# Performance work log

Hardware: AMD Instinct MI355X
Metric: run time of the kernel (lower is better)

## Reference

```python
import jax, jax.numpy as jnp
import numpy as np

BATCH, C, IMG, P = 32, 3, 224, 32
G = IMG // P            # 7
N = G * G               # 49 patches
E, NH, L = 768, 12, 12
DH = E // NH
DFF, MLP, NC = 3072, 2048, 5
FLAT = (N + 1 + L) * E  # 62*768 = 47616


def setup_inputs() -> dict:
    key = jax.random.key(0)
    ks = iter(jax.random.split(key, 32))
    nrm = lambda shape, s=0.02: jax.random.normal(next(ks), shape, jnp.float32) * s
    return {
        "x": jax.random.normal(next(ks), (BATCH, C, IMG, IMG), jnp.float32),
        "Wp": nrm((E, C, P, P)), "bp": jnp.zeros((E,), jnp.float32),
        "cls_token": jnp.zeros((1, 1, E), jnp.float32),
        "pos_embed": nrm((E, G + 1, G + 1)),  # overwritten by normal init in torch code
        "W_bb": nrm((C, E)), "b_bb": jnp.zeros((E,), jnp.float32),
        "Wqkv": nrm((L, 3 * E, E)), "bqkv": jnp.zeros((L, 3 * E), jnp.float32),
        "Wo": nrm((L, E, E)), "bo": jnp.zeros((L, E), jnp.float32),
        "ln1_s": jnp.ones((L, E), jnp.float32), "ln1_b": jnp.zeros((L, E), jnp.float32),
        "W1": nrm((L, DFF, E)), "b1": jnp.zeros((L, DFF), jnp.float32),
        "W2": nrm((L, E, DFF)), "b2": jnp.zeros((L, E), jnp.float32),
        "ln2_s": jnp.ones((L, E), jnp.float32), "ln2_b": jnp.zeros((L, E), jnp.float32),
        "lnf_s": jnp.ones((E,), jnp.float32), "lnf_b": jnp.zeros((E,), jnp.float32),
        "Wh1": nrm((MLP, FLAT)), "bh1": jnp.zeros((MLP,), jnp.float32),
        "Wh2": nrm((NC, MLP)), "bh2": jnp.zeros((NC,), jnp.float32),
    }


def _ln(x, s, b, eps=1e-5):
    mu = x.mean(-1, keepdims=True)
    var = ((x - mu) ** 2).mean(-1, keepdims=True)
    return (x - mu) * jax.lax.rsqrt(var + eps) * s + b


def reference(x, Wp, bp, cls_token, pos_embed, W_bb, b_bb,
              Wqkv, bqkv, Wo, bo, ln1_s, ln1_b, W1, b1, W2, b2, ln2_s, ln2_b,
              lnf_s, lnf_b, Wh1, bh1, Wh2, bh2):
    B = x.shape[0]
    # backbone stub: global average pool + linear -> [B, E]
    ximg = x.mean((2, 3)) @ W_bb + b_bb
    # patch embedding (importance weights are all ones -> subdivision branch is dead;
    # equivalent to strided conv, row-major patch order)
    xr = x.reshape(B, C, G, P, G, P)
    emb = jnp.einsum('bcipjq,ecpq->beij', xr, Wp) + bp[None, :, None, None]  # [B,E,G,G]
    patches = emb.reshape(B, E, N).transpose(0, 2, 1)                       # [B,N,E]
    h = jnp.concatenate([jnp.broadcast_to(cls_token, (B, 1, E)), patches], axis=1)
    pe = pos_embed.reshape(1, -1, E)[:, :h.shape[1], :]
    h = h + pe
    inv_sqrt_dh = 1.0 / np.sqrt(DH)
    for i in range(L):  # post-norm transformer encoder layer (relu FFN), seq grows each iter
        S = h.shape[1]
        qkv = h @ Wqkv[i].T + bqkv[i]
        q, k, v = jnp.split(qkv, 3, axis=-1)
        q = q.reshape(B, S, NH, DH)
        k = k.reshape(B, S, NH, DH)
        v = v.reshape(B, S, NH, DH)
        att = jax.nn.softmax(jnp.einsum('bqhd,bkhd->bhqk', q, k) * inv_sqrt_dh, axis=-1)
        o = jnp.einsum('bhqk,bkhd->bqhd', att, v).reshape(B, S, E) @ Wo[i].T + bo[i]
        h = _ln(h + o, ln1_s[i], ln1_b[i])
        ff = jax.nn.relu(h @ W1[i].T + b1[i]) @ W2[i].T + b2[i]
        h = _ln(h + ff, ln2_s[i], ln2_b[i])
        h = jnp.concatenate([ximg[:, None, :], h], axis=1)  # prepend backbone token
    h = _ln(h, lnf_s, lnf_b)
    h = h.reshape(B, -1)  # [B, (N+1+L)*E]
    out = jax.nn.gelu(h @ Wh1.T + bh1, approximate=False) @ Wh2.T + bh2
    return out
```

## Files before the change

kernel.cpp:

```cpp
#include <hip/hip_runtime.h>
#include <math.h>

#define B_ 32
#define C_ 3
#define IMG_ 224
#define P_ 32
#define G_ 7
#define NPATCH 49
#define E_ 768
#define NH_ 12
#define L_ 12
#define DFF_ 3072
#define MLP_ 2048
#define NC_ 5
#define TOK 62
#define MROWS (B_*TOK)
#define FLAT_ (TOK*E_)
#define MPAD 2048
#define PMROWS (B_*NPATCH)
#define PMPAD 1664
#define HKS 31
#define HKC (FLAT_/HKS)

#define WQKV_SZ (2304*768)
#define WO_SZ   (768*768)
#define W1_SZ   (3072*768)
#define W2_SZ   (768*3072)

typedef __bf16 bf16x8 __attribute__((ext_vector_type(8)));
typedef float f32x4 __attribute__((ext_vector_type(4)));

__device__ inline unsigned short f2bf(float f) {
    unsigned u = __float_as_uint(f);
    u += 0x7FFF + ((u >> 16) & 1);
    return (unsigned short)(u >> 16);
}

__device__ inline unsigned cvtpk(float lo, float hi) {
    unsigned r;
    asm("v_cvt_pk_bf16_f32 %0, %1, %2" : "=v"(r) : "v"(lo), "v"(hi));
    return r;
}

#define GLDS(gsrc, ldst) __builtin_amdgcn_global_load_lds( \
    (__attribute__((address_space(1))) const void*)(gsrc), \
    (__attribute__((address_space(3))) void*)(ldst), 16, 0, 0)

__global__ __launch_bounds__(256) void cvt_kernel(
    const float* __restrict__ in, unsigned short* __restrict__ out, int n4)
{
    int i = blockIdx.x * 256 + threadIdx.x;
    if (i >= n4) return;
    float4 v = reinterpret_cast<const float4*>(in)[i];
    ushort4 o;
    o.x = f2bf(v.x); o.y = f2bf(v.y); o.z = f2bf(v.z); o.w = f2bf(v.w);
    reinterpret_cast<ushort4*>(out)[i] = o;
}

__global__ __launch_bounds__(256) void gemm_mfma(
    const unsigned short* __restrict__ A, const unsigned short* __restrict__ W,
    const float* __restrict__ bias, float* __restrict__ Cf, unsigned short* __restrict__ Cb,
    float* __restrict__ part, int M, int N, int K, int KC, int act)
{
    __shared__ unsigned short As[128 * 64];
    __shared__ unsigned short Bs[128 * 64];
    int tid = threadIdx.x;
    int m0 = blockIdx.y * 128, n0 = blockIdx.x * 128;
    int z = blockIdx.z;
    int kbeg = z * KC;
    int wid = tid >> 6, lane = tid & 63;
    int wm = wid >> 1, wn = wid & 1;
    int lr = lane & 15, lg = lane >> 4;
    int sr = tid >> 3, sc = (tid & 7) * 8;

    f32x4 acc[4][4];
    #pragma unroll
    for (int mi = 0; mi < 4; ++mi)
        #pragma unroll
        for (int ni = 0; ni < 4; ++ni)
            acc[mi][ni] = (f32x4){0.f, 0.f, 0.f, 0.f};

    for (int k0 = kbeg; k0 < kbeg + KC; k0 += 64) {
        #pragma unroll
        for (int t = 0; t < 4; ++t)
            GLDS(&A[(size_t)(m0 + sr + t * 32) * K + k0 + sc], &As[(sr + t * 32) * 64 + sc]);
        #pragma unroll
        for (int t = 0; t < 4; ++t)
            GLDS(&W[(size_t)(n0 + sr + t * 32) * K + k0 + sc], &Bs[(sr + t * 32) * 64 + sc]);
        __syncthreads();
        #pragma unroll
        for (int ks = 0; ks < 64; ks += 32) {
            bf16x8 af[4], bfr[4];
            #pragma unroll
            for (int mi = 0; mi < 4; ++mi)
                af[mi] = *reinterpret_cast<const bf16x8*>(&As[(wm * 64 + mi * 16 + lr) * 64 + ks + lg * 8]);
            #pragma unroll
            for (int ni = 0; ni < 4; ++ni)
                bfr[ni] = *reinterpret_cast<const bf16x8*>(&Bs[(wn * 64 + ni * 16 + lr) * 64 + ks + lg * 8]);
            #pragma unroll
            for (int mi = 0; mi < 4; ++mi)
                #pragma unroll
                for (int ni = 0; ni < 4; ++ni)
                    acc[mi][ni] = __builtin_amdgcn_mfma_f32_16x16x32_bf16(af[mi], bfr[ni], acc[mi][ni], 0, 0, 0);
        }
        __syncthreads();
    }

    bool split = (gridDim.z > 1);
    #pragma unroll
    for (int mi = 0; mi < 4; ++mi) {
        #pragma unroll
        for (int rr = 0; rr < 4; ++rr) {
            int row = m0 + wm * 64 + mi * 16 + lg * 4 + rr;
            #pragma unroll
            for (int ni = 0; ni < 4; ++ni) {
                int col = n0 + wn * 64 + ni * 16 + lr;
                float v = acc[mi][ni][rr];
                if (split) {
                    part[((size_t)z * M + row) * N + col] = v;
                } else {
                    v += bias[col];
                    if (act) v = fmaxf(v, 0.f);
                    if (Cb) Cb[(size_t)row * N + col] = f2bf(v);
                    else    Cf[(size_t)row * N + col] = v;
                }
            }
        }
    }
}

__global__ __launch_bounds__(256) void add_ln_fused(
    const float* __restrict__ h, const float* __restrict__ part, int nparts,
    const float* __restrict__ gb, const float* __restrict__ s, const float* __restrict__ bb,
    float* __restrict__ outf, unsigned short* __restrict__ outbf,
    const float* __restrict__ ximg, int tnew)
{
    int row = blockIdx.x;
    int t = row % TOK, b = row / TOK;
    int tid = threadIdx.x;
    if (t == tnew) {
        #pragma unroll
        for (int j = 0; j < 3; ++j) {
            int e = tid + j * 256;
            float v = ximg[b * E_ + e];
            if (outf)  outf[(size_t)row * E_ + e] = v;
            if (outbf) outbf[(size_t)row * E_ + e] = f2bf(v);
        }
        return;
    }
    __shared__ float sm[8];
    float v[3];
    #pragma unroll
    for (int j = 0; j < 3; ++j) {
        int e = tid + j * 256;
        float x = h[(size_t)row * E_ + e];
        for (int p = 0; p < nparts; ++p) x += part[((size_t)p * MPAD + row) * E_ + e];
        if (nparts) x += gb[e];
        v[j] = x;
    }
    float sum = v[0] + v[1] + v[2];
    #pragma unroll
    for (int o = 32; o >= 1; o >>= 1) sum += __shfl_xor(sum, o);
    int wid = tid >> 6, lane = tid & 63;
    if (lane == 0) sm[wid] = sum;
    __syncthreads();
    if (tid == 0) sm[0] = sm[0] + sm[1] + sm[2] + sm[3];
    __syncthreads();
    float mu = sm[0] * (1.0f / E_);
    __syncthreads();
    float sq = 0.f;
    #pragma unroll
    for (int j = 0; j < 3; ++j) { float d = v[j] - mu; sq += d * d; }
    #pragma unroll
    for (int o = 32; o >= 1; o >>= 1) sq += __shfl_xor(sq, o);
    if (lane == 0) sm[wid] = sq;
    __syncthreads();
    if (tid == 0) sm[0] = sm[0] + sm[1] + sm[2] + sm[3];
    __syncthreads();
    float rstd = rsqrtf(sm[0] * (1.0f / E_) + 1e-5f);
    #pragma unroll
    for (int j = 0; j < 3; ++j) {
        int e = tid + j * 256;
        float r = (v[j] - mu) * rstd * s[e] + bb[e];
        if (outf)  outf[(size_t)row * E_ + e] = r;
        if (outbf) outbf[(size_t)row * E_ + e] = f2bf(r);
    }
}

__global__ __launch_bounds__(256) void attn_mfma(
    const unsigned short* __restrict__ qkv, unsigned short* __restrict__ obf, int start)
{
    int h = blockIdx.x, b = blockIdx.y;
    int S = TOK - start;
    int tid = threadIdx.x;
    int wid = tid >> 6, lane = tid & 63;
    int lr = lane & 15, lg = lane >> 4;

    __shared__ unsigned short Qs[64 * 64];
    __shared__ unsigned short Ks[64 * 64];
    __shared__ unsigned short VT[64 * 72];
    __shared__ unsigned short Ps[4][16 * 72];

    const unsigned short* base = qkv + ((size_t)(b * TOK + start)) * 2304 + h * 64;

    #pragma unroll
    for (int t = 0; t < 2; ++t) {
        int r0 = wid * 16 + t * 8;
        int row = r0 + (lane >> 3);
        int sc = ((lane & 7) ^ (row & 7)) * 8;
        GLDS(base + (size_t)row * 2304 + sc,       &Qs[r0 * 64]);
        GLDS(base + (size_t)row * 2304 + 768 + sc, &Ks[r0 * 64]);
    }
    #pragma unroll
    for (int it = 0; it < 8; ++it) {
        int pi = it * 256 + tid;
        int k = pi >> 5;
        int d0 = (pi & 31) * 2;
        unsigned u = *reinterpret_cast<const unsigned*>(base + (size_t)k * 2304 + 1536 + d0);
        VT[d0 * 72 + k] = (unsigned short)(u & 0xffff);
        VT[(d0 + 1) * 72 + k] = (unsigned short)(u >> 16);
    }
    __syncthreads();

    f32x4 st[4];
    #pragma unroll
    for (int mt = 0; mt < 4; ++mt) st[mt] = (f32x4){0.f, 0.f, 0.f, 0.f};
    bf16x8 qb[2];
    #pragma unroll
    for (int ks = 0; ks < 2; ++ks) {
        int qrow = wid * 16 + lr;
        int ck = ((ks * 4 + lg) ^ (qrow & 7)) * 8;
        qb[ks] = *reinterpret_cast<const bf16x8*>(&Qs[qrow * 64 + ck]);
    }
    #pragma unroll
    for (int mt = 0; mt < 4; ++mt) {
        #pragma unroll
        for (int ks = 0; ks < 2; ++ks) {
            int krow = mt * 16 + lr;
            int ck = ((ks * 4 + lg) ^ (krow & 7)) * 8;
            bf16x8 kb = *reinterpret_cast<const bf16x8*>(&Ks[krow * 64 + ck]);
            st[mt] = __builtin_amdgcn_mfma_f32_16x16x32_bf16(kb, qb[ks], st[mt], 0, 0, 0);
        }
    }

    float mx = -1e30f;
    #pragma unroll
    for (int mt = 0; mt < 4; ++mt)
        #pragma unroll
        for (int rr = 0; rr < 4; ++rr) {
            int k = mt * 16 + lg * 4 + rr;
            float v = st[mt][rr] * 0.125f;
            v = (k < S) ? v : -1e30f;
            st[mt][rr] = v;
            mx = fmaxf(mx, v);
        }
    mx = fmaxf(mx, __shfl_xor(mx, 16));
    mx = fmaxf(mx, __shfl_xor(mx, 32));
    float sum = 0.f;
    #pragma unroll
    for (int mt = 0; mt < 4; ++mt)
        #pragma unroll
        for (int rr = 0; rr < 4; ++rr) {
            float p = __expf(st[mt][rr] - mx);
            st[mt][rr] = p;
            sum += p;
        }
    sum += __shfl_xor(sum, 16);
    sum += __shfl_xor(sum, 32);
    float inv = 1.0f / sum;

    #pragma unroll
    for (int mt = 0; mt < 4; ++mt) {
        int k0 = mt * 16 + lg * 4;
        unsigned u0 = cvtpk(st[mt][0] * inv, st[mt][1] * inv);
        unsigned u1 = cvtpk(st[mt][2] * inv, st[mt][3] * inv);
        *reinterpret_cast<unsigned*>(&Ps[wid][lr * 72 + k0]) = u0;
        *reinterpret_cast<unsigned*>(&Ps[wid][lr * 72 + k0 + 2]) = u1;
    }
    __syncthreads();

    f32x4 oa[4];
    #pragma unroll
    for (int nt = 0; nt < 4; ++nt) oa[nt] = (f32x4){0.f, 0.f, 0.f, 0.f};
    #pragma unroll
    for (int ks = 0; ks < 2; ++ks) {
        bf16x8 pa = *reinterpret_cast<const bf16x8*>(&Ps[wid][lr * 72 + ks * 32 + lg * 8]);
        #pragma unroll
        for (int nt = 0; nt < 4; ++nt) {
            bf16x8 vb = *reinterpret_cast<const bf16x8*>(&VT[(nt * 16 + lr) * 72 + ks * 32 + lg * 8]);
            oa[nt] = __builtin_amdgcn_mfma_f32_16x16x32_bf16(pa, vb, oa[nt], 0, 0, 0);
        }
    }

    #pragma unroll
    for (int nt = 0; nt < 4; ++nt)
        #pragma unroll
        for (int rr = 0; rr < 4; ++rr) {
            int qs = wid * 16 + lg * 4 + rr;
            if (qs < S)
                obf[((size_t)(b * TOK + start + qs)) * E_ + h * 64 + nt * 16 + lr] = f2bf(oa[nt][rr]);
        }
}

__global__ __launch_bounds__(256) void mean_kernel(const float* __restrict__ x, float* __restrict__ xmean)
{
    int bc = blockIdx.x;
    const float* p = x + (size_t)bc * IMG_ * IMG_;
    float s = 0.f;
    for (int i = threadIdx.x; i < IMG_ * IMG_; i += 256) s += p[i];
    #pragma unroll
    for (int o = 32; o >= 1; o >>= 1) s += __shfl_xor(s, o);
    __shared__ float sm[4];
    int wid = threadIdx.x >> 6, lane = threadIdx.x & 63;
    if (lane == 0) sm[wid] = s;
    __syncthreads();
    if (threadIdx.x == 0) xmean[bc] = (sm[0] + sm[1] + sm[2] + sm[3]) / (float)(IMG_ * IMG_);
}

__global__ void ximg_kernel(const float* __restrict__ xmean, const float* __restrict__ Wbb,
                            const float* __restrict__ bbb, float* __restrict__ ximg)
{
    int idx = blockIdx.x * 256 + threadIdx.x;
    if (idx >= B_ * E_) return;
    int e = idx % E_, b = idx / E_;
    ximg[idx] = xmean[b * 3 + 0] * Wbb[0 * E_ + e]
              + xmean[b * 3 + 1] * Wbb[1 * E_ + e]
              + xmean[b * 3 + 2] * Wbb[2 * E_ + e] + bbb[e];
}

__global__ void im2col_kernel(const float* __restrict__ x, unsigned short* __restrict__ Pm)
{
    int idx = blockIdx.x * 256 + threadIdx.x;
    if (idx >= PMROWS * 3072) return;
    int k = idx % 3072;
    int rowp = idx / 3072;
    int n = rowp % NPATCH, b = rowp / NPATCH;
    int i = n / G_, j = n % G_;
    int c = k >> 10;
    int r = k & 1023;
    int p = r >> 5, q = r & 31;
    Pm[idx] = f2bf(x[(((size_t)b * C_ + c) * IMG_ + i * P_ + p) * IMG_ + j * P_ + q]);
}

__global__ void build_h0_kernel(const float* __restrict__ part, const float* __restrict__ bp,
                                const float* __restrict__ cls, const float* __restrict__ pos,
                                float* __restrict__ hbuf, unsigned short* __restrict__ hbf)
{
    int idx = blockIdx.x * 256 + threadIdx.x;
    if (idx >= MROWS * E_) return;
    int e = idx % E_;
    int t = (idx / E_) % TOK;
    int b = idx / (E_ * TOK);
    float v = 0.f;
    if (t >= 12) {
        int sseq = t - 12;
        float base;
        if (sseq == 0) base = cls[e];
        else {
            int prow = b * NPATCH + (sseq - 1);
            base = bp[e];
            #pragma unroll
            for (int s = 0; s < 3; ++s) base += part[((size_t)s * PMPAD + prow) * E_ + e];
        }
        v = base + pos[sseq * E_ + e];
    }
    hbuf[idx] = v;
    hbf[idx] = f2bf(v);
}

__global__ __launch_bounds__(256) void head1_mfma(
    const unsigned short* __restrict__ hfb, const float* __restrict__ Wh1,
    float* __restrict__ part)
{
    int tid = threadIdx.x;
    int wid = tid >> 6, lane = tid & 63;
    int lr = lane & 15, lg = lane >> 4;
    int n0 = blockIdx.x * 64 + wid * 16;
    int kc = blockIdx.y;
    f32x4 acc0 = (f32x4){0.f, 0.f, 0.f, 0.f};
    f32x4 acc1 = (f32x4){0.f, 0.f, 0.f, 0.f};
    const float* wrow = Wh1 + (size_t)(n0 + lr) * FLAT_ + (size_t)kc * HKC + lg * 8;
    const unsigned short* a0 = hfb + (size_t)lr * FLAT_ + (size_t)kc * HKC + lg * 8;
    const unsigned short* a1 = hfb + (size_t)(16 + lr) * FLAT_ + (size_t)kc * HKC + lg * 8;
    #pragma unroll 4
    for (int k = 0; k < HKC; k += 32) {
        float4 w0 = *reinterpret_cast<const float4*>(wrow + k);
        float4 w1 = *reinterpret_cast<const float4*>(wrow + k + 4);
        uint4 u;
        u.x = cvtpk(w0.x, w0.y); u.y = cvtpk(w0.z, w0.w);
        u.z = cvtpk(w1.x, w1.y); u.w = cvtpk(w1.z, w1.w);
        bf16x8 bw = __builtin_bit_cast(bf16x8, u);
        bf16x8 af0 = *reinterpret_cast<const bf16x8*>(a0 + k);
        bf16x8 af1 = *reinterpret_cast<const bf16x8*>(a1 + k);
        acc0 = __builtin_amdgcn_mfma_f32_16x16x32_bf16(af0, bw, acc0, 0, 0, 0);
        acc1 = __builtin_amdgcn_mfma_f32_16x16x32_bf16(af1, bw, acc1, 0, 0, 0);
    }
    int n = n0 + lr;
    #pragma unroll
    for (int rr = 0; rr < 4; ++rr) {
        int m = lg * 4 + rr;
        part[((size_t)kc * B_ + m) * MLP_ + n] = acc0[rr];
        part[((size_t)kc * B_ + 16 + m) * MLP_ + n] = acc1[rr];
    }
}

__global__ void head1_fin_kernel(const float* __restrict__ part, const float* __restrict__ bh1,
                                 float* __restrict__ out1)
{
    int idx = blockIdx.x * 256 + threadIdx.x;
    if (idx >= B_ * MLP_) return;
    int n = idx % MLP_, b = idx / MLP_;
    float s = bh1[n];
    for (int kc = 0; kc < HKS; ++kc) s += part[((size_t)kc * B_ + b) * MLP_ + n];
    out1[idx] = 0.5f * s * (1.0f + erff(s * 0.70710678118654752f));
}

__global__ __launch_bounds__(256) void head2_kernel(const float* __restrict__ out1,
                                                    const float* __restrict__ Wh2,
                                                    const float* __restrict__ bh2,
                                                    float* __restrict__ out)
{
    int bc = blockIdx.x;
    int b = bc / NC_, c = bc % NC_;
    float s = 0.f;
    for (int nn = threadIdx.x; nn < MLP_; nn += 256) s += out1[(size_t)b * MLP_ + nn] * Wh2[(size_t)c * MLP_ + nn];
    #pragma unroll
    for (int o = 32; o >= 1; o >>= 1) s += __shfl_xor(s, o);
    __shared__ float sm[4];
    int wid = threadIdx.x >> 6, lane = threadIdx.x & 63;
    if (lane == 0) sm[wid] = s;
    __syncthreads();
    if (threadIdx.x == 0) out[bc] = sm[0] + sm[1] + sm[2] + sm[3] + bh2[c];
}

extern "C" void kernel_launch(void* const* d_in, const int* in_sizes, int n_in,
                              void* d_out, int out_size, void* d_ws, size_t ws_size,
                              hipStream_t stream)
{
    (void)in_sizes; (void)n_in; (void)out_size; (void)ws_size;
    const float* x    = (const float*)d_in[0];
    const float* Wp   = (const float*)d_in[1];
    const float* bp   = (const float*)d_in[2];
    const float* cls  = (const float*)d_in[3];
    const float* pos  = (const float*)d_in[4];
    const float* Wbb  = (const float*)d_in[5];
    const float* bbb  = (const float*)d_in[6];
    const float* Wqkv = (const float*)d_in[7];
    const float* bqkv = (const float*)d_in[8];
    const float* Wo   = (const float*)d_in[9];
    const float* bo   = (const float*)d_in[10];
    const float* ln1s = (const float*)d_in[11];
    const float* ln1b = (const float*)d_in[12];
    const float* W1   = (const float*)d_in[13];
    const float* b1   = (const float*)d_in[14];
    const float* W2   = (const float*)d_in[15];
    const float* b2   = (const float*)d_in[16];
    const float* ln2s = (const float*)d_in[17];
    const float* ln2b = (const float*)d_in[18];
    const float* lnfs = (const float*)d_in[19];
    const float* lnfb = (const float*)d_in[20];
    const float* Wh1  = (const float*)d_in[21];
    const float* bh1  = (const float*)d_in[22];
    const float* Wh2  = (const float*)d_in[23];
    const float* bh2  = (const float*)d_in[24];
    float* out = (float*)d_out;

    float* ws = (float*)d_ws;
    size_t off = 0;
    float* hbuf   = ws + off; off += (size_t)MROWS * E_;
    float* qslab  = ws + off; off += (size_t)3 * MPAD * E_;
    unsigned short* hbf  = (unsigned short*)(ws + off); off += (size_t)MPAD * E_ / 2;
    unsigned short* obf  = (unsigned short*)(ws + off); off += (size_t)MPAD * E_ / 2;
    unsigned short* ffbf = (unsigned short*)(ws + off); off += (size_t)MPAD * DFF_ / 2;
    unsigned short* wqb  = (unsigned short*)(ws + off); off += (size_t)L_ * WQKV_SZ / 2;
    unsigned short* wob  = (unsigned short*)(ws + off); off += (size_t)L_ * WO_SZ / 2;
    unsigned short* w1b  = (unsigned short*)(ws + off); off += (size_t)L_ * W1_SZ / 2;
    unsigned short* w2b  = (unsigned short*)(ws + off); off += (size_t)L_ * W2_SZ / 2;
    unsigned short* wpb  = (unsigned short*)(ws + off); off += (size_t)E_ * 3072 / 2;
    unsigned short* hfb  = (unsigned short*)(ws + off); off += (size_t)MROWS * E_ / 2;
    float* ximg  = ws + off; off += B_ * E_;
    float* xmean = ws + off; off += 128;
    float* out1  = ws + off; off += B_ * MLP_;

    float* part = qslab;
    unsigned short* qkvb = (unsigned short*)qslab;
    unsigned short* Pmbf = ffbf;

    cvt_kernel<<<(L_ * WQKV_SZ / 4 + 255) / 256, 256, 0, stream>>>(Wqkv, wqb, L_ * WQKV_SZ / 4);
    cvt_kernel<<<(L_ * WO_SZ / 4 + 255) / 256, 256, 0, stream>>>(Wo, wob, L_ * WO_SZ / 4);
    cvt_kernel<<<(L_ * W1_SZ / 4 + 255) / 256, 256, 0, stream>>>(W1, w1b, L_ * W1_SZ / 4);
    cvt_kernel<<<(L_ * W2_SZ / 4 + 255) / 256, 256, 0, stream>>>(W2, w2b, L_ * W2_SZ / 4);
    cvt_kernel<<<(E_ * 3072 / 4 + 255) / 256, 256, 0, stream>>>(Wp, wpb, E_ * 3072 / 4);

    mean_kernel<<<B_ * C_, 256, 0, stream>>>(x, xmean);
    ximg_kernel<<<(B_ * E_ + 255) / 256, 256, 0, stream>>>(xmean, Wbb, bbb, ximg);

    im2col_kernel<<<(PMROWS * 3072 + 255) / 256, 256, 0, stream>>>(x, Pmbf);
    gemm_mfma<<<dim3(E_ / 128, PMPAD / 128, 3), 256, 0, stream>>>(
        Pmbf, wpb, nullptr, nullptr, nullptr, part, PMPAD, E_, 3072, 1024, 0);
    build_h0_kernel<<<(MROWS * E_ + 255) / 256, 256, 0, stream>>>(part, bp, cls, pos, hbuf, hbf);

    for (int i = 0; i < L_; ++i) {
        int start = 12 - i;
        gemm_mfma<<<dim3(2304 / 128, MPAD / 128, 1), 256, 0, stream>>>(
            hbf, wqb + (size_t)i * WQKV_SZ, bqkv + i * 2304, nullptr, qkvb, nullptr, MPAD, 2304, E_, E_, 0);
        attn_mfma<<<dim3(NH_, B_), 256, 0, stream>>>(qkvb, obf, start);
        gemm_mfma<<<dim3(E_ / 128, MPAD / 128, 3), 256, 0, stream>>>(
            obf, wob + (size_t)i * WO_SZ, nullptr, nullptr, nullptr, part, MPAD, E_, E_, 256, 0);
        add_ln_fused<<<MROWS, 256, 0, stream>>>(
            hbuf, part, 3, bo + i * E_, ln1s + i * E_, ln1b + i * E_, hbuf, hbf, nullptr, -1);
        gemm_mfma<<<dim3(DFF_ / 128, MPAD / 128, 1), 256, 0, stream>>>(
            hbf, w1b + (size_t)i * W1_SZ, b1 + i * DFF_, nullptr, ffbf, nullptr, MPAD, DFF_, E_, E_, 1);
        gemm_mfma<<<dim3(E_ / 128, MPAD / 128, 3), 256, 0, stream>>>(
            ffbf, w2b + (size_t)i * W2_SZ, nullptr, nullptr, nullptr, part, MPAD, E_, DFF_, 1024, 0);
        add_ln_fused<<<MROWS, 256, 0, stream>>>(
            hbuf, part, 3, b2 + i * E_, ln2s + i * E_, ln2b + i * E_, hbuf, hbf, ximg, 11 - i);
    }

    add_ln_fused<<<MROWS, 256, 0, stream>>>(
        hbuf, nullptr, 0, nullptr, lnfs, lnfb, nullptr, hfb, nullptr, -1);
    head1_mfma<<<dim3(MLP_ / 64, HKS), 256, 0, stream>>>(hfb, Wh1, part);
    head1_fin_kernel<<<(B_ * MLP_ + 255) / 256, 256, 0, stream>>>(part, bh1, out1);
    head2_kernel<<<B_ * NC_, 256, 0, stream>>>(out1, Wh2, bh2, out);
}
```

Before: 1.980 ms.

## Fuse fp32-to-bf16 weight conversion into GEMM loads and remap workgroups per XCD

Removes the separate weight conversion kernels. The GEMM now loads fp32 weights directly into registers and converts them to bf16 while storing to LDS, which avoids writing and re-reading a full bf16 copy of every layer's weights. It also remaps workgroup IDs so neighbouring tiles land on the same XCD for better L2 reuse, and vectorises im2col to four elements per thread. In exchange, each weight tile is fetched at double width by every M-tile block, and the loads go through registers instead of direct-to-LDS.

```diff
diff --git a/kernel.cpp b/kernel.cpp
--- a/kernel.cpp
+++ b/kernel.cpp
@@ -22,11 +22,6 @@
 #define HKS 31
 #define HKC (FLAT_/HKS)
 
-#define WQKV_SZ (2304*768)
-#define WO_SZ   (768*768)
-#define W1_SZ   (3072*768)
-#define W2_SZ   (768*3072)
-
 typedef __bf16 bf16x8 __attribute__((ext_vector_type(8)));
 typedef float f32x4 __attribute__((ext_vector_type(4)));
 
@@ -46,26 +41,23 @@
     (__attribute__((address_space(1))) const void*)(gsrc), \
     (__attribute__((address_space(3))) void*)(ldst), 16, 0, 0)
 
-__global__ __launch_bounds__(256) void cvt_kernel(
-    const float* __restrict__ in, unsigned short* __restrict__ out, int n4)
-{
-    int i = blockIdx.x * 256 + threadIdx.x;
-    if (i >= n4) return;
-    float4 v = reinterpret_cast<const float4*>(in)[i];
-    ushort4 o;
-    o.x = f2bf(v.x); o.y = f2bf(v.y); o.z = f2bf(v.z); o.w = f2bf(v.w);
-    reinterpret_cast<ushort4*>(out)[i] = o;
-}
-
 __global__ __launch_bounds__(256) void gemm_mfma(
-    const unsigned short* __restrict__ A, const unsigned short* __restrict__ W,
+    const unsigned short* __restrict__ A, const float* __restrict__ W,
     const float* __restrict__ bias, float* __restrict__ Cf, unsigned short* __restrict__ Cb,
     float* __restrict__ part, int M, int N, int K, int KC, int act)
 {
     __shared__ unsigned short As[128 * 64];
     __shared__ unsigned short Bs[128 * 64];
     int tid = threadIdx.x;
-    int m0 = blockIdx.y * 128, n0 = blockIdx.x * 128;
+
+    int gx = gridDim.x;
+    int nwg = gx * gridDim.y;
+    int lid = blockIdx.y * gx + blockIdx.x;
+    int qq = nwg >> 3, rr8 = nwg & 7;
+    int xcd = lid & 7, sidx = lid >> 3;
+    int wg = (xcd < rr8 ? xcd * (qq + 1) : rr8 * (qq + 1) + (xcd - rr8) * qq) + sidx;
+    int m0 = (wg / gx) * 128, n0 = (wg % gx) * 128;
+
     int z = blockIdx.z;
     int kbeg = z * KC;
     int wid = tid >> 6, lane = tid & 63;
@@ -81,12 +73,27 @@
             acc[mi][ni] = (f32x4){0.f, 0.f, 0.f, 0.f};
 
     for (int k0 = kbeg; k0 < kbeg + KC; k0 += 64) {
+        float4 wv[4][2];
+        #pragma unroll
+        for (int t = 0; t < 4; ++t) {
+            int ci = t * 256 + tid;
+            int r = ci >> 3, c8 = (ci & 7) * 8;
+            const float* src = &W[(size_t)(n0 + r) * K + k0 + c8];
+            wv[t][0] = *reinterpret_cast<const float4*>(src);
+            wv[t][1] = *reinterpret_cast<const float4*>(src + 4);
+        }
         #pragma unroll
         for (int t = 0; t < 4; ++t)
             GLDS(&A[(size_t)(m0 + sr + t * 32) * K + k0 + sc], &As[(sr + t * 32) * 64 + sc]);
         #pragma unroll
-        for (int t = 0; t < 4; ++t)
-            GLDS(&W[(size_t)(n0 + sr + t * 32) * K + k0 + sc], &Bs[(sr + t * 32) * 64 + sc]);
+        for (int t = 0; t < 4; ++t) {
+            int ci = t * 256 + tid;
+            int r = ci >> 3, c8 = (ci & 7) * 8;
+            uint4 u;
+            u.x = cvtpk(wv[t][0].x, wv[t][0].y); u.y = cvtpk(wv[t][0].z, wv[t][0].w);
+            u.z = cvtpk(wv[t][1].x, wv[t][1].y); u.w = cvtpk(wv[t][1].z, wv[t][1].w);
+            *reinterpret_cast<uint4*>(&Bs[r * 64 + c8]) = u;
+        }
         __syncthreads();
         #pragma unroll
         for (int ks = 0; ks < 64; ks += 32) {
@@ -330,7 +337,7 @@
 
 __global__ void im2col_kernel(const float* __restrict__ x, unsigned short* __restrict__ Pm)
 {
-    int idx = blockIdx.x * 256 + threadIdx.x;
+    int idx = (blockIdx.x * 256 + threadIdx.x) * 4;
     if (idx >= PMROWS * 3072) return;
     int k = idx % 3072;
     int rowp = idx / 3072;
@@ -339,7 +346,11 @@
     int c = k >> 10;
     int r = k & 1023;
     int p = r >> 5, q = r & 31;
-    Pm[idx] = f2bf(x[(((size_t)b * C_ + c) * IMG_ + i * P_ + p) * IMG_ + j * P_ + q]);
+    float4 v = *reinterpret_cast<const float4*>(
+        &x[(((size_t)b * C_ + c) * IMG_ + i * P_ + p) * IMG_ + j * P_ + q]);
+    ushort4 o;
+    o.x = f2bf(v.x); o.y = f2bf(v.y); o.z = f2bf(v.z); o.w = f2bf(v.w);
+    *reinterpret_cast<ushort4*>(&Pm[idx]) = o;
 }
 
 __global__ void build_h0_kernel(const float* __restrict__ part, const float* __restrict__ bp,
@@ -472,11 +483,6 @@
     unsigned short* hbf  = (unsigned short*)(ws + off); off += (size_t)MPAD * E_ / 2;
     unsigned short* obf  = (unsigned short*)(ws + off); off += (size_t)MPAD * E_ / 2;
     unsigned short* ffbf = (unsigned short*)(ws + off); off += (size_t)MPAD * DFF_ / 2;
-    unsigned short* wqb  = (unsigned short*)(ws + off); off += (size_t)L_ * WQKV_SZ / 2;
-    unsigned short* wob  = (unsigned short*)(ws + off); off += (size_t)L_ * WO_SZ / 2;
-    unsigned short* w1b  = (unsigned short*)(ws + off); off += (size_t)L_ * W1_SZ / 2;
-    unsigned short* w2b  = (unsigned short*)(ws + off); off += (size_t)L_ * W2_SZ / 2;
-    unsigned short* wpb  = (unsigned short*)(ws + off); off += (size_t)E_ * 3072 / 2;
     unsigned short* hfb  = (unsigned short*)(ws + off); off += (size_t)MROWS * E_ / 2;
     float* ximg  = ws + off; off += B_ * E_;
     float* xmean = ws + off; off += 128;
@@ -486,33 +492,27 @@
     unsigned short* qkvb = (unsigned short*)qslab;
     unsigned short* Pmbf = ffbf;
 
-    cvt_kernel<<<(L_ * WQKV_SZ / 4 + 255) / 256, 256, 0, stream>>>(Wqkv, wqb, L_ * WQKV_SZ / 4);
-    cvt_kernel<<<(L_ * WO_SZ / 4 + 255) / 256, 256, 0, stream>>>(Wo, wob, L_ * WO_SZ / 4);
-    cvt_kernel<<<(L_ * W1_SZ / 4 + 255) / 256, 256, 0, stream>>>(W1, w1b, L_ * W1_SZ / 4);
-    cvt_kernel<<<(L_ * W2_SZ / 4 + 255) / 256, 256, 0, stream>>>(W2, w2b, L_ * W2_SZ / 4);
-    cvt_kernel<<<(E_ * 3072 / 4 + 255) / 256, 256, 0, stream>>>(Wp, wpb, E_ * 3072 / 4);
-
     mean_kernel<<<B_ * C_, 256, 0, stream>>>(x, xmean);
     ximg_kernel<<<(B_ * E_ + 255) / 256, 256, 0, stream>>>(xmean, Wbb, bbb, ximg);
 
-    im2col_kernel<<<(PMROWS * 3072 + 255) / 256, 256, 0, stream>>>(x, Pmbf);
+    im2col_kernel<<<(PMROWS * 3072 / 4 + 255) / 256, 256, 0, stream>>>(x, Pmbf);
     gemm_mfma<<<dim3(E_ / 128, PMPAD / 128, 3), 256, 0, stream>>>(
-        Pmbf, wpb, nullptr, nullptr, nullptr, part, PMPAD, E_, 3072, 1024, 0);
+        Pmbf, Wp, nullptr, nullptr, nullptr, part, PMPAD, E_, 3072, 1024, 0);
     build_h0_kernel<<<(MROWS * E_ + 255) / 256, 256, 0, stream>>>(part, bp, cls, pos, hbuf, hbf);
 
     for (int i = 0; i < L_; ++i) {
         int start = 12 - i;
         gemm_mfma<<<dim3(2304 / 128, MPAD / 128, 1), 256, 0, stream>>>(
-            hbf, wqb + (size_t)i * WQKV_SZ, bqkv + i * 2304, nullptr, qkvb, nullptr, MPAD, 2304, E_, E_, 0);
+            hbf, Wqkv + (size_t)i * 2304 * E_, bqkv + i * 2304, nullptr, qkvb, nullptr, MPAD, 2304, E_, E_, 0);
         attn_mfma<<<dim3(NH_, B_), 256, 0, stream>>>(qkvb, obf, start);
         gemm_mfma<<<dim3(E_ / 128, MPAD / 128, 3), 256, 0, stream>>>(
-            obf, wob + (size_t)i * WO_SZ, nullptr, nullptr, nullptr, part, MPAD, E_, E_, 256, 0);
+            obf, Wo + (size_t)i * E_ * E_, nullptr, nullptr, nullptr, part, MPAD, E_, E_, 256, 0);
         add_ln_fused<<<MROWS, 256, 0, stream>>>(
             hbuf, part, 3, bo + i * E_, ln1s + i * E_, ln1b + i * E_, hbuf, hbf, nullptr, -1);
         gemm_mfma<<<dim3(DFF_ / 128, MPAD / 128, 1), 256, 0, stream>>>(
-            hbf, w1b + (size_t)i * W1_SZ, b1 + i * DFF_, nullptr, ffbf, nullptr, MPAD, DFF_, E_, E_, 1);
+            hbf, W1 + (size_t)i * DFF_ * E_, b1 + i * DFF_, nullptr, ffbf, nullptr, MPAD, DFF_, E_, E_, 1);
         gemm_mfma<<<dim3(E_ / 128, MPAD / 128, 3), 256, 0, stream>>>(
-            ffbf, w2b + (size_t)i * W2_SZ, nullptr, nullptr, nullptr, part, MPAD, E_, DFF_, 1024, 0);
+            ffbf, W2 + (size_t)i * E_ * DFF_, nullptr, nullptr, nullptr, part, MPAD, E_, DFF_, 1024, 0);
         add_ln_fused<<<MROWS, 256, 0, stream>>>(
             hbuf, part, 3, b2 + i * E_, ln2s + i * E_, ln2b + i * E_, hbuf, hbf, ximg, 11 - i);
     }
```

Result: slower. 2.163 ms (+9.2%).
